# Performance work log

Hardware: AMD Instinct MI355X
Metric: run time of the kernel (lower is better)

## Reference

```python
import jax, jax.numpy as jnp
import numpy as np

EMBED = 1024
HEADS = 16
HEAD_DIM = EMBED // HEADS
N, L = 2, 2048


def setup_inputs() -> dict:
    key = jax.random.key(0)
    ks = jax.random.split(key, 9)
    s = 0.02
    return {
        "values": jax.random.normal(ks[0], (N, L, EMBED), jnp.float32),
        "key": jax.random.normal(ks[1], (N, L, EMBED), jnp.float32),
        "query": jax.random.normal(ks[2], (N, L, EMBED), jnp.float32),
        "mask": jnp.ones((N, 1, 1, L), jnp.int32),
        "Wv": jax.random.normal(ks[3], (HEAD_DIM, HEAD_DIM), jnp.float32) * s,
        "Wk": jax.random.normal(ks[4], (HEAD_DIM, HEAD_DIM), jnp.float32) * s,
        "Wq": jax.random.normal(ks[5], (HEAD_DIM, HEAD_DIM), jnp.float32) * s,
        "bq": jax.random.normal(ks[6], (HEAD_DIM,), jnp.float32) * s,
        "Wo": jax.random.normal(ks[7], (EMBED, EMBED), jnp.float32) * s,
        "bo": jax.random.normal(ks[8], (EMBED,), jnp.float32) * s,
    }


def reference(values, key, query, mask, Wv, Wk, Wq, bq, Wo, bo):
    n, q_len, E = query.shape
    D = Wv.shape[0]
    H = E // D
    # split heads: (N, len, H, D)
    v = values.reshape(n, -1, H, D)
    k = key.reshape(n, -1, H, D)
    q = query.reshape(n, q_len, H, D)
    # per-head linear projections (torch Linear: x @ W.T [+ b])
    v = jnp.einsum("nlhd,ed->nlhe", v, Wv)
    k = jnp.einsum("nlhd,ed->nlhe", k, Wk)
    q = jnp.einsum("nlhd,ed->nlhe", q, Wq) + bq
    # scores: (N, H, q_len, k_len)
    energy = jnp.einsum("nqhd,nkhd->nhqk", q, k)
    energy = jnp.where(mask == 0, jnp.float32(-1e20), energy)
    # NOTE: original scales by sqrt(embed_size), not sqrt(head_dim)
    attn = jax.nn.softmax(energy / jnp.sqrt(jnp.float32(E)), axis=-1)
    out = jnp.einsum("nhqk,nkhd->nqhd", attn, v).reshape(n, q_len, E)
    return out @ Wo.T + bo
```

## Files before the change

### kernel.cpp

```cpp
#include <hip/hip_runtime.h>
#include <hip/hip_bf16.h>
#include <string.h>

#define NB   2
#define SEQ  2048
#define EMB  1024
#define NH   16
#define HD   64
#define QSCALE 0.045084219f
#define MADD2  -4.5084219e18f

typedef __attribute__((ext_vector_type(8))) short short8;
typedef __attribute__((ext_vector_type(4))) float f32x4;

#define MFMA(a, b, c) __builtin_amdgcn_mfma_f32_16x16x32_bf16(a, b, c, 0, 0, 0)
#define EXP2(x) __builtin_amdgcn_exp2f(x)

__device__ __forceinline__ unsigned short f2bf(float x) {
    union { float f; unsigned u; } v; v.f = x;
    unsigned r = v.u + 0x7fffu + ((v.u >> 16) & 1u);
    return (unsigned short)(r >> 16);
}
__device__ __forceinline__ unsigned packbf2(float a, float b) {
    __hip_bfloat162 h = __float22bfloat162_rn(make_float2(a, b));
    unsigned u; memcpy(&u, &h, 4);
    return u;
}

__global__ __launch_bounds__(256) void cvt_kernel(
    const float* __restrict__ Wo, const float* __restrict__ Wq,
    const float* __restrict__ Wk, const float* __restrict__ Wv,
    const int* __restrict__ mask,
    unsigned short* __restrict__ Wob, unsigned short* __restrict__ Wqb,
    unsigned short* __restrict__ Wkb, unsigned short* __restrict__ Wvb,
    float* __restrict__ maddG)
{
    const int b = blockIdx.x, tid = threadIdx.x;
    if (b < 1024) {
        int idx = b * 256 + tid;
        float4 w = ((const float4*)Wo)[idx];
        uint2 p; p.x = packbf2(w.x, w.y); p.y = packbf2(w.z, w.w);
        ((uint2*)Wob)[idx] = p;
    } else if (b < 1027) {
        const float* W = (b == 1024) ? Wq : (b == 1025) ? Wk : Wv;
        unsigned short* Wb = (b == 1024) ? Wqb : (b == 1025) ? Wkb : Wvb;
        #pragma unroll
        for (int i = 0; i < 4; ++i) {
            int idx = tid + i * 256;
            float4 w = ((const float4*)W)[idx];
            uint2 p; p.x = packbf2(w.x, w.y); p.y = packbf2(w.z, w.w);
            ((uint2*)Wb)[idx] = p;
        }
    } else {
        #pragma unroll
        for (int i = 0; i < 16; ++i) {
            int idx = tid + i * 256;
            maddG[idx] = mask[idx] ? 0.f : MADD2;
        }
    }
}

__global__ __launch_bounds__(256) void qkv_kernel(
    const float* __restrict__ Qin, const float* __restrict__ Kin,
    const float* __restrict__ Vin,
    const unsigned short* __restrict__ Wqb, const unsigned short* __restrict__ Wkb,
    const unsigned short* __restrict__ Wvb, const float* __restrict__ bq,
    unsigned short* __restrict__ Qp, unsigned short* __restrict__ Kp,
    unsigned short* __restrict__ Vtp)
{
    const int lt = blockIdx.x;
    const int h  = blockIdx.y;
    const int tz = blockIdx.z;
    const int t  = tz >> 1, n = tz & 1;

    const float* X; const unsigned short* Wb;
    if (t == 0)      { X = Qin; Wb = Wqb; }
    else if (t == 1) { X = Kin; Wb = Wkb; }
    else             { X = Vin; Wb = Wvb; }

    __shared__ __align__(16) unsigned short sX[128][70];
    __shared__ __align__(16) unsigned short sT[64][136];

    const int tid = threadIdx.x, wave = tid >> 6, lane = tid & 63;
    const int ln = lane & 15, quad = lane >> 4;

    #pragma unroll
    for (int i = 0; i < 8; ++i) {
        int flat = tid + i * 256;
        int r = flat >> 4, c4 = flat & 15;
        float4 xv = *(const float4*)(X + ((size_t)(n * SEQ + lt * 128 + r)) * EMB + h * HD + c4 * 4);
        uint2 xp; xp.x = packbf2(xv.x, xv.y); xp.y = packbf2(xv.z, xv.w);
        *(uint2*)&sX[r][c4 * 4] = xp;
    }
    short8 wf0[4], wf1[4];
    #pragma unroll
    for (int nt = 0; nt < 4; ++nt) {
        wf0[nt] = *(const short8*)(Wb + (nt * 16 + ln) * HD + quad * 8);
        wf1[nt] = *(const short8*)(Wb + (nt * 16 + ln) * HD + 32 + quad * 8);
    }
    __syncthreads();

    f32x4 acc[2][4];
    #pragma unroll
    for (int set = 0; set < 2; ++set) {
        short8 af0 = *(const short8*)&sX[wave * 32 + set * 16 + ln][quad * 8];
        short8 af1 = *(const short8*)&sX[wave * 32 + set * 16 + ln][32 + quad * 8];
        #pragma unroll
        for (int nt = 0; nt < 4; ++nt) {
            f32x4 a = {0.f, 0.f, 0.f, 0.f};
            a = MFMA(af0, wf0[nt], a);
            a = MFMA(af1, wf1[nt], a);
            acc[set][nt] = a;
        }
    }

    if (t == 0) {
        #pragma unroll
        for (int nt = 0; nt < 4; ++nt) {
            float bb = bq[nt * 16 + ln];
            #pragma unroll
            for (int set = 0; set < 2; ++set)
                #pragma unroll
                for (int a = 0; a < 4; ++a)
                    acc[set][nt][a] = (acc[set][nt][a] + bb) * QSCALE;
        }
    }

    if (t < 2) {
        unsigned short* Out = (t == 0) ? Qp : Kp;
        #pragma unroll
        for (int set = 0; set < 2; ++set)
            #pragma unroll
            for (int a = 0; a < 4; ++a) {
                size_t row = (size_t)((n * NH + h) * SEQ + lt * 128 + wave * 32 + set * 16 + quad * 4 + a);
                #pragma unroll
                for (int nt = 0; nt < 4; ++nt)
                    Out[row * HD + nt * 16 + ln] = f2bf(acc[set][nt][a]);
            }
    } else {
        #pragma unroll
        for (int set = 0; set < 2; ++set)
            #pragma unroll
            for (int nt = 0; nt < 4; ++nt)
                #pragma unroll
                for (int a = 0; a < 4; ++a)
                    sT[nt * 16 + ln][wave * 32 + set * 16 + quad * 4 + a] = f2bf(acc[set][nt][a]);
        __syncthreads();
        #pragma unroll
        for (int i = 0; i < 4; ++i) {
            int flat = tid + i * 256;
            int r = flat >> 4, c8 = flat & 15;
            *(float4*)(Vtp + ((size_t)((n * NH + h) * HD + r)) * SEQ + lt * 128 + c8 * 8) =
                *(const float4*)&sT[r][c8 * 8];
        }
    }
}

__global__ __launch_bounds__(128, 2) void flash_kernel(
    const unsigned short* __restrict__ Qp, const unsigned short* __restrict__ Kp,
    const unsigned short* __restrict__ Vtp, const float* __restrict__ maddG,
    unsigned short* __restrict__ A )
{
    const int nh = blockIdx.x;
    const int qt = blockIdx.y;
    const int n  = nh >> 4, h = nh & 15;

    const int tid  = threadIdx.x;
    const int wave = tid >> 6, lane = tid & 63;
    const int ln   = lane & 15, quad = lane >> 4;

    __shared__ __align__(16) unsigned short sP[2][64][72];
    float (*xO)[65] = reinterpret_cast<float(*)[65]>(&sP[0][0][0]);
    float* xl = reinterpret_cast<float*>(reinterpret_cast<char*>(&sP[0][0][0]) + 64 * 65 * 4);

    const unsigned short* Qb = Qp + ((size_t)nh * SEQ + qt * 64) * HD;
    short8 qf[4][2];
    #pragma unroll
    for (int set = 0; set < 4; ++set) {
        qf[set][0] = *(const short8*)(Qb + (set * 16 + ln) * HD + quad * 8);
        qf[set][1] = *(const short8*)(Qb + (set * 16 + ln) * HD + 32 + quad * 8);
    }

    const unsigned short* Kb = Kp  + (size_t)nh * SEQ * HD;
    const unsigned short* Vb = Vtp + (size_t)nh * HD * SEQ;
    const float* mb = maddG + n * SEQ;

    f32x4 o[4][4];
    #pragma unroll
    for (int s2 = 0; s2 < 4; ++s2)
        #pragma unroll
        for (int dt = 0; dt < 4; ++dt) o[s2][dt] = (f32x4){0.f, 0.f, 0.f, 0.f};
    float lsum[4] = {0.f, 0.f, 0.f, 0.f};

    const int kt0 = wave * (SEQ / 64 / 2);
    for (int kt = kt0; kt < kt0 + SEQ / 64 / 2; ++kt) {
        short8 vf[4][2];
        #pragma unroll
        for (int dt = 0; dt < 4; ++dt) {
            const unsigned short* vr = Vb + (size_t)(dt * 16 + ln) * SEQ + kt * 64;
            vf[dt][0] = *(const short8*)(vr + quad * 8);
            vf[dt][1] = *(const short8*)(vr + 32 + quad * 8);
        }

        #pragma unroll
        for (int nt = 0; nt < 4; ++nt) {
            const unsigned short* kr = Kb + (size_t)(kt * 64 + nt * 16 + ln) * HD;
            short8 kf0 = *(const short8*)(kr + quad * 8);
            short8 kf1 = *(const short8*)(kr + 32 + quad * 8);
            float4 md  = *(const float4*)(mb + kt * 64 + nt * 16 + quad * 4);

            #pragma unroll
            for (int set = 0; set < 4; ++set) {
                f32x4 z = {0.f, 0.f, 0.f, 0.f};
                z = MFMA(kf0, qf[set][0], z);
                z = MFMA(kf1, qf[set][1], z);
                float p0 = EXP2(fminf(z[0] + md.x, 80.f));
                float p1 = EXP2(fminf(z[1] + md.y, 80.f));
                float p2 = EXP2(fminf(z[2] + md.z, 80.f));
                float p3 = EXP2(fminf(z[3] + md.w, 80.f));
                lsum[set] += (p0 + p1) + (p2 + p3);
                uint2 w; w.x = packbf2(p0, p1); w.y = packbf2(p2, p3);
                *(uint2*)&sP[wave][set * 16 + ln][nt * 16 + quad * 4] = w;
            }
        }
        asm volatile("s_waitcnt lgkmcnt(0)" ::: "memory");

        #pragma unroll
        for (int set = 0; set < 4; ++set) {
            short8 pf0 = *(const short8*)&sP[wave][set * 16 + ln][quad * 8];
            short8 pf1 = *(const short8*)&sP[wave][set * 16 + ln][32 + quad * 8];
            #pragma unroll
            for (int dt = 0; dt < 4; ++dt) {
                o[set][dt] = MFMA(pf0, vf[dt][0], o[set][dt]);
                o[set][dt] = MFMA(pf1, vf[dt][1], o[set][dt]);
            }
        }
    }

    float lf[4];
    #pragma unroll
    for (int set = 0; set < 4; ++set) {
        float l = lsum[set];
        l += __shfl_xor(l, 16);
        l += __shfl_xor(l, 32);
        lf[set] = l;
    }

    __syncthreads();
    if (wave == 1) {
        #pragma unroll
        for (int set = 0; set < 4; ++set) {
            #pragma unroll
            for (int a = 0; a < 4; ++a)
                #pragma unroll
                for (int dt = 0; dt < 4; ++dt)
                    xO[set * 16 + quad * 4 + a][dt * 16 + ln] = o[set][dt][a];
            if (quad == 0) xl[set * 16 + ln] = lf[set];
        }
    }
    __syncthreads();
    if (wave == 0) {
        #pragma unroll
        for (int set = 0; set < 4; ++set)
            #pragma unroll
            for (int a = 0; a < 4; ++a) {
                int q = set * 16 + quad * 4 + a;
                float l0 = __shfl(lf[set], q & 15);
                float inv = 1.0f / (l0 + xl[q]);
                size_t row = (size_t)(n * SEQ + qt * 64 + q);
                #pragma unroll
                for (int dt = 0; dt < 4; ++dt)
                    A[row * EMB + h * HD + dt * 16 + ln] =
                        f2bf((o[set][dt][a] + xO[q][dt * 16 + ln]) * inv);
            }
    }
}

__global__ __launch_bounds__(256) void outproj_kernel(
    const unsigned short* __restrict__ A, const unsigned short* __restrict__ Wob,
    const float* __restrict__ bo, float* __restrict__ Out)
{
    const int ct = blockIdx.x;
    const int rt = blockIdx.y;

    const int tid  = threadIdx.x;
    const int wave = tid >> 6, lane = tid & 63;
    const int ln   = lane & 15, quad = lane >> 4;
    const int wm   = wave >> 1, wn = wave & 1;

    __shared__ __align__(16) unsigned short sA[128][72];
    __shared__ __align__(16) unsigned short sB[128][72];

    f32x4 acc[4][4];
    #pragma unroll
    for (int i = 0; i < 4; ++i)
        #pragma unroll
        for (int j = 0; j < 4; ++j) acc[i][j] = (f32x4){0.f, 0.f, 0.f, 0.f};

    for (int kc = 0; kc < EMB / 64; ++kc) {
        __syncthreads();
        #pragma unroll
        for (int i = 0; i < 4; ++i) {
            int flat = tid + i * 256;
            int r = flat >> 3, c8 = flat & 7;
            *(float4*)&sA[r][c8 * 8] =
                *(const float4*)(A + (size_t)(rt * 128 + r) * EMB + kc * 64 + c8 * 8);
            *(float4*)&sB[r][c8 * 8] =
                *(const float4*)(Wob + (size_t)(ct * 128 + r) * EMB + kc * 64 + c8 * 8);
        }
        __syncthreads();

        #pragma unroll
        for (int ks = 0; ks < 2; ++ks) {
            short8 af[4], bf[4];
            #pragma unroll
            for (int i = 0; i < 4; ++i)
                af[i] = *(const short8*)&sA[wm * 64 + i * 16 + ln][ks * 32 + quad * 8];
            #pragma unroll
            for (int j = 0; j < 4; ++j)
                bf[j] = *(const short8*)&sB[wn * 64 + j * 16 + ln][ks * 32 + quad * 8];
            #pragma unroll
            for (int i = 0; i < 4; ++i)
                #pragma unroll
                for (int j = 0; j < 4; ++j)
                    acc[i][j] = MFMA(af[i], bf[j], acc[i][j]);
        }
    }

    #pragma unroll
    for (int j = 0; j < 4; ++j) {
        int col = ct * 128 + wn * 64 + j * 16 + ln;
        float bb = bo[col];
        #pragma unroll
        for (int i = 0; i < 4; ++i)
            #pragma unroll
            for (int a = 0; a < 4; ++a) {
                size_t row = (size_t)(rt * 128 + wm * 64 + i * 16 + quad * 4 + a);
                Out[row * EMB + col] = acc[i][j][a] + bb;
            }
    }
}

extern "C" void kernel_launch(void* const* d_in, const int* in_sizes, int n_in,
                              void* d_out, int out_size, void* d_ws, size_t ws_size,
                              hipStream_t stream) {
    const float* values = (const float*)d_in[0];
    const float* key_   = (const float*)d_in[1];
    const float* query  = (const float*)d_in[2];
    const int*   mask   = (const int*)d_in[3];
    const float* Wv     = (const float*)d_in[4];
    const float* Wk     = (const float*)d_in[5];
    const float* Wq     = (const float*)d_in[6];
    const float* bq     = (const float*)d_in[7];
    const float* Wo     = (const float*)d_in[8];
    const float* bo     = (const float*)d_in[9];
    float* out = (float*)d_out;

    const size_t NHLD = (size_t)NB * NH * SEQ * HD;

    unsigned short* ws = (unsigned short*)d_ws;
    unsigned short* Qp    = ws;
    unsigned short* Kp    = ws + NHLD;
    unsigned short* Vtp   = ws + 2 * NHLD;
    unsigned short* Aattn = ws + 3 * NHLD;
    unsigned short* Wob   = ws + 4 * NHLD;
    unsigned short* Wqb   = Wob + (size_t)EMB * EMB;
    unsigned short* Wkb   = Wqb + HD * HD;
    unsigned short* Wvb   = Wkb + HD * HD;
    float* maddG = (float*)(Wvb + HD * HD);

    cvt_kernel<<<dim3(1028), 256, 0, stream>>>(
        Wo, Wq, Wk, Wv, mask, Wob, Wqb, Wkb, Wvb, maddG);
    qkv_kernel<<<dim3(SEQ / 128, NH, 3 * NB), 256, 0, stream>>>(
        query, key_, values, Wqb, Wkb, Wvb, bq, Qp, Kp, Vtp);
    flash_kernel<<<dim3(NB * NH, SEQ / 64), 128, 0, stream>>>(
        Qp, Kp, Vtp, maddG, Aattn);
    outproj_kernel<<<dim3(EMB / 128, NB * SEQ / 128), 256, 0, stream>>>(
        Aattn, Wob, bo, out);
}
```

Measured before the change: 212.8 us.

## Split flash attention key range across four waves with two-stage reduction

Each flash block now runs four waves instead of two, and each wave covers a quarter of the key tiles rather than half. The partial outputs and row sums are combined in shared memory in two steps: waves 2 and 3 hand their partials to waves 0 and 1, then wave 1 hands its result to wave 0. The aim is more resident waves per CU to hide memory and MFMA latency, and a shorter serial key loop per wave. In exchange it adds extra shared-memory traffic and barriers. The tighter launch bound of 256 threads with 4 blocks may also limit VGPRs enough to cause spills.

```diff
diff --git a/kernel.cpp b/kernel.cpp
--- a/kernel.cpp
+++ b/kernel.cpp
@@ -156,7 +156,7 @@
     }
 }
 
-__global__ __launch_bounds__(128, 2) void flash_kernel(
+__global__ __launch_bounds__(256, 4) void flash_kernel(
     const unsigned short* __restrict__ Qp, const unsigned short* __restrict__ Kp,
     const unsigned short* __restrict__ Vtp, const float* __restrict__ maddG,
     unsigned short* __restrict__ A )
@@ -169,9 +169,9 @@
     const int wave = tid >> 6, lane = tid & 63;
     const int ln   = lane & 15, quad = lane >> 4;
 
-    __shared__ __align__(16) unsigned short sP[2][64][72];
-    float (*xO)[65] = reinterpret_cast<float(*)[65]>(&sP[0][0][0]);
-    float* xl = reinterpret_cast<float*>(reinterpret_cast<char*>(&sP[0][0][0]) + 64 * 65 * 4);
+    __shared__ __align__(16) unsigned short sP[4][64][72];
+    float (*xO)[64][65] = reinterpret_cast<float(*)[64][65]>(&sP[0][0][0]);
+    float* xl = reinterpret_cast<float*>(reinterpret_cast<char*>(&sP[0][0][0]) + 2 * 64 * 65 * 4);
 
     const unsigned short* Qb = Qp + ((size_t)nh * SEQ + qt * 64) * HD;
     short8 qf[4][2];
@@ -192,8 +192,8 @@
         for (int dt = 0; dt < 4; ++dt) o[s2][dt] = (f32x4){0.f, 0.f, 0.f, 0.f};
     float lsum[4] = {0.f, 0.f, 0.f, 0.f};
 
-    const int kt0 = wave * (SEQ / 64 / 2);
-    for (int kt = kt0; kt < kt0 + SEQ / 64 / 2; ++kt) {
+    const int kt0 = wave * (SEQ / 64 / 4);
+    for (int kt = kt0; kt < kt0 + SEQ / 64 / 4; ++kt) {
         short8 vf[4][2];
         #pragma unroll
         for (int dt = 0; dt < 4; ++dt) {
@@ -247,6 +247,31 @@
     }
 
     __syncthreads();
+    if (wave >= 2) {
+        const int slot = wave - 2;
+        #pragma unroll
+        for (int set = 0; set < 4; ++set) {
+            #pragma unroll
+            for (int a = 0; a < 4; ++a)
+                #pragma unroll
+                for (int dt = 0; dt < 4; ++dt)
+                    xO[slot][set * 16 + quad * 4 + a][dt * 16 + ln] = o[set][dt][a];
+            if (quad == 0) xl[slot * 64 + set * 16 + ln] = lf[set];
+        }
+    }
+    __syncthreads();
+    if (wave < 2) {
+        #pragma unroll
+        for (int set = 0; set < 4; ++set) {
+            #pragma unroll
+            for (int a = 0; a < 4; ++a)
+                #pragma unroll
+                for (int dt = 0; dt < 4; ++dt)
+                    o[set][dt][a] += xO[wave][set * 16 + quad * 4 + a][dt * 16 + ln];
+            lf[set] += xl[wave * 64 + set * 16 + ln];
+        }
+    }
+    __syncthreads();
     if (wave == 1) {
         #pragma unroll
         for (int set = 0; set < 4; ++set) {
@@ -254,7 +279,7 @@
             for (int a = 0; a < 4; ++a)
                 #pragma unroll
                 for (int dt = 0; dt < 4; ++dt)
-                    xO[set * 16 + quad * 4 + a][dt * 16 + ln] = o[set][dt][a];
+                    xO[0][set * 16 + quad * 4 + a][dt * 16 + ln] = o[set][dt][a];
             if (quad == 0) xl[set * 16 + ln] = lf[set];
         }
     }
@@ -271,7 +296,7 @@
                 #pragma unroll
                 for (int dt = 0; dt < 4; ++dt)
                     A[row * EMB + h * HD + dt * 16 + ln] =
-                        f2bf((o[set][dt][a] + xO[q][dt * 16 + ln]) * inv);
+                        f2bf((o[set][dt][a] + xO[0][q][dt * 16 + ln]) * inv);
             }
     }
 }
@@ -373,7 +398,7 @@
         Wo, Wq, Wk, Wv, mask, Wob, Wqb, Wkb, Wvb, maddG);
     qkv_kernel<<<dim3(SEQ / 128, NH, 3 * NB), 256, 0, stream>>>(
         query, key_, values, Wqb, Wkb, Wvb, bq, Qp, Kp, Vtp);
-    flash_kernel<<<dim3(NB * NH, SEQ / 64), 128, 0, stream>>>(
+    flash_kernel<<<dim3(NB * NH, SEQ / 64), 256, 0, stream>>>(
         Qp, Kp, Vtp, maddG, Aattn);
     outproj_kernel<<<dim3(EMB / 128, NB * SEQ / 128), 256, 0, stream>>>(
         Aattn, Wob, bo, out);
```

Result: slower. 463.6 us (+117.9%).
